# Kernel tuning notes

Hardware: AMD Instinct MI355X
Metric: run time of the kernel (lower is better)

The kernel has to match this reference:

```python
import jax, jax.numpy as jnp
import numpy as np

D_MODEL = 1024
D_KV = 64
N_HEADS = 16
KV_HEADS = 4
G = N_HEADS // KV_HEADS
NUM_BUCKETS = 32
MAX_DISTANCE = 128


def _relative_position_bucket(relative_position, bidirectional=True,
                              num_buckets=NUM_BUCKETS, max_distance=MAX_DISTANCE):
    # Faithful port of T5Attention._relative_position_bucket
    relative_buckets = jnp.zeros_like(relative_position)
    if bidirectional:
        num_buckets //= 2
        relative_buckets = (relative_position > 0).astype(jnp.int32) * num_buckets
        relative_position = jnp.abs(relative_position)
    else:
        relative_position = -jnp.minimum(relative_position, 0)
    max_exact = num_buckets // 2
    is_small = relative_position < max_exact
    rel_if_large = max_exact + (
        jnp.log(relative_position.astype(jnp.float32) / max_exact)
        / np.log(max_distance / max_exact) * (num_buckets - max_exact)
    ).astype(jnp.int32)
    rel_if_large = jnp.minimum(rel_if_large, num_buckets - 1)
    return relative_buckets + jnp.where(is_small, relative_position, rel_if_large)


def setup_inputs() -> dict:
    key = jax.random.key(0)
    ks = jax.random.split(key, 6)
    B, S = 2, 2048
    inner = N_HEADS * D_KV
    sc = 1.0 / np.sqrt(D_MODEL)
    return {
        "hidden_states": jax.random.normal(ks[0], (B, S, D_MODEL), dtype=jnp.float32),
        "Wq": jax.random.normal(ks[1], (D_MODEL, inner), dtype=jnp.float32) * sc,
        "Wk": jax.random.normal(ks[2], (D_MODEL, inner), dtype=jnp.float32) * sc,
        "Wv": jax.random.normal(ks[3], (D_MODEL, inner), dtype=jnp.float32) * sc,
        "Wo": jax.random.normal(ks[4], (inner, D_MODEL), dtype=jnp.float32) * sc,
        "rel_bias": jax.random.normal(ks[5], (NUM_BUCKETS, N_HEADS), dtype=jnp.float32) * 0.1,
    }


def reference(hidden_states, Wq, Wk, Wv, Wo, rel_bias):
    B, S, _ = hidden_states.shape

    def split_heads(x):  # [B,S,inner] -> [B,H,S,Dk]
        return x.reshape(B, S, N_HEADS, D_KV).transpose(0, 2, 1, 3)

    q = split_heads(hidden_states @ Wq)
    k = split_heads(hidden_states @ Wk)
    v = split_heads(hidden_states @ Wv)

    # head index = g * KV_HEADS + h (einops 'b (g h) ...' with h=kv_heads)
    gq = q.reshape(B, G, KV_HEADS, S, D_KV)
    gk = k.reshape(B, G, KV_HEADS, S, D_KV).mean(axis=1)  # [B,Hkv,S,Dk]
    # einsum sums over g (as in torch.einsum 'bghnd,bhsd->bhns'); no 1/sqrt(d) in T5
    scores = jnp.einsum('bghnd,bhsd->bhns', gq, gk)  # [B,Hkv,S,S]

    # T5 relative position bias (bidirectional, encoder)
    ctx = jnp.arange(S)[:, None]
    mem = jnp.arange(S)[None, :]
    buckets = _relative_position_bucket(mem - ctx, bidirectional=True)
    bias = rel_bias[buckets]                # [S,S,H]
    bias = bias.transpose(2, 0, 1)[None]    # [1,H,S,S]
    gbias = bias.reshape(1, G, KV_HEADS, S, S).mean(axis=1)  # [1,Hkv,S,S]

    scores = scores + gbias
    attn = jax.nn.softmax(scores.astype(jnp.float32), axis=-1).astype(scores.dtype)

    # repeat grouped attn weights back to full heads: 'b h n s -> b (g h) n s'
    attn_full = jnp.tile(attn, (1, G, 1, 1))  # [B,H,S,S]
    ctx_out = jnp.einsum('bhns,bhsd->bhnd', attn_full, v)  # [B,H,S,Dk]
    ctx_out = ctx_out.transpose(0, 2, 1, 3).reshape(B, S, N_HEADS * D_KV)
    return ctx_out @ Wo  # [B,S,D_MODEL]
```

## Files before the change

kernel.cpp:

```cpp
#include <hip/hip_runtime.h>
#include <math.h>


typedef __bf16 bf16_t;
typedef bf16_t bf16x8 __attribute__((ext_vector_type(8)));
typedef bf16_t bf16x4 __attribute__((ext_vector_type(4)));
typedef float f32x4 __attribute__((ext_vector_type(4)));

#define MFMA16(a, b, c) __builtin_amdgcn_mfma_f32_16x16x32_bf16(a, b, c, 0, 0, 0)

typedef __attribute__((address_space(1))) void gvoid;
typedef __attribute__((address_space(3))) void svoid;
__device__ __forceinline__ void gld16(const void* g, void* l) {
    __builtin_amdgcn_global_load_lds((gvoid*)g, (svoid*)l, 16, 0, 0);
}

__global__ __launch_bounds__(256) void prep_all(const float* __restrict__ hs,
                                                const float* __restrict__ Wq,
                                                const float* __restrict__ Wk,
                                                const float* __restrict__ Wv,
                                                const float* __restrict__ Wo,
                                                const float* __restrict__ rel_bias,
                                                bf16_t* __restrict__ hs_hi,
                                                bf16_t* __restrict__ hs_lo,
                                                bf16_t* __restrict__ Thi,
                                                bf16_t* __restrict__ Tlo,
                                                bf16_t* __restrict__ WvT,
                                                bf16_t* __restrict__ WoT,
                                                float* __restrict__ btab) {
    __shared__ float sm[2048];
    const int r = blockIdx.x, t = threadIdx.x;
    if (r < 4096) {
        size_t idx = ((size_t)r * 256 + t) * 4;
        float4 v = *(const float4*)(hs + idx);
        bf16x4 h, l;
        h[0] = (bf16_t)v.x; l[0] = (bf16_t)(v.x - (float)h[0]);
        h[1] = (bf16_t)v.y; l[1] = (bf16_t)(v.y - (float)h[1]);
        h[2] = (bf16_t)v.z; l[2] = (bf16_t)(v.z - (float)h[2]);
        h[3] = (bf16_t)v.w; l[3] = (bf16_t)(v.w - (float)h[3]);
        *(bf16x4*)(hs_hi + idx) = h;
        *(bf16x4*)(hs_lo + idx) = l;
    } else if (r < 5120) {
        int k = r - 4096;
        float* rq = sm;
        float* rk = sm + 1024;
#pragma unroll
        for (int j = 0; j < 4; ++j) {
            rq[t + j * 256] = Wq[(size_t)k * 1024 + t + j * 256];
            rk[t + j * 256] = Wk[(size_t)k * 1024 + t + j * 256];
        }
        __syncthreads();
        int h = t >> 6, j2 = t & 63;
        float sq = 0.f, sk = 0.f;
#pragma unroll
        for (int g = 0; g < 4; ++g) {
            sq += rq[(g * 4 + h) * 64 + j2];
            sk += rk[(g * 4 + h) * 64 + j2];
        }
        sk *= 0.25f;
        bf16_t qh = (bf16_t)sq;
        Thi[(size_t)t * 1024 + k] = qh;
        Tlo[(size_t)t * 1024 + k] = (bf16_t)(sq - (float)qh);
        bf16_t kh = (bf16_t)sk;
        Thi[(size_t)(256 + t) * 1024 + k] = kh;
        Tlo[(size_t)(256 + t) * 1024 + k] = (bf16_t)(sk - (float)kh);
    } else if (r < 7168) {
        const float* src = (r < 6144) ? Wv : Wo;
        bf16_t* dst = (r < 6144) ? WvT : WoT;
        int rr = (r < 6144) ? r - 5120 : r - 6144;
        int bx = (rr & 31) * 32, by = (rr >> 5) * 32;
        int tx = t & 31, ty = t >> 5;
        float(*tile)[33] = (float(*)[33])sm;
#pragma unroll
        for (int i = 0; i < 32; i += 8)
            tile[ty + i][tx] = src[(size_t)(by + ty + i) * 1024 + bx + tx];
        __syncthreads();
#pragma unroll
        for (int i = 0; i < 32; i += 8)
            dst[(size_t)(bx + ty + i) * 1024 + by + tx] = (bf16_t)tile[tx][ty + i];
    } else {
        int idx = (r - 7168) * 256 + t;
        if (idx >= 4095) return;
        int delta = idx - 2047;
        int bucket = (delta > 0) ? 16 : 0;
        int arp = delta < 0 ? -delta : delta;
        int rb;
        if (arp < 8) {
            rb = arp;
        } else {
            float tt = (logf((float)arp * 0.125f) / 2.772588722239781f) * 8.0f;
            int ri = 8 + (int)tt;
            rb = ri < 15 ? ri : 15;
        }
        bucket += rb;
#pragma unroll
        for (int h = 0; h < 4; ++h) {
            float s = 0.25f * (rel_bias[bucket * 16 + h] + rel_bias[bucket * 16 + h + 4] +
                               rel_bias[bucket * 16 + h + 8] + rel_bias[bucket * 16 + h + 12]);
            btab[h * 4608 + idx] = s;
        }
    }
}

__global__ __launch_bounds__(256, 1) void proj_qkv(const bf16_t* __restrict__ Ah,
                                                   const bf16_t* __restrict__ Al,
                                                   const bf16_t* __restrict__ Bh,
                                                   const bf16_t* __restrict__ Bl,
                                                   const bf16_t* __restrict__ WvT,
                                                   bf16_t* __restrict__ Qhi,
                                                   bf16_t* __restrict__ Qlo,
                                                   bf16_t* __restrict__ Kbh,
                                                   bf16_t* __restrict__ Kbl,
                                                   bf16_t* __restrict__ Vb) {
    __shared__ bf16_t pool[24576];
    const int K = 1024, nk = 32;
    const int t = threadIdx.x;
    const int w = t >> 6, lane = t & 63;
    const int lr = lane & 15, q = lane >> 4;
    const int bx = blockIdx.x;
    const bool qk = bx < 8;
    const int m0 = blockIdx.y * 128;
    const int n0 = qk ? bx * 64 : (bx - 8) * 128;
    const int mw = (w & 1) * 64;
    f32x4 acc[4][4] = {};

    const int rA = t & 127, cA0 = t >> 7, cA1 = 2 + (t >> 7);
    const size_t oA0 = (size_t)(m0 + rA) * K + cA0 * 8;
    const size_t oA1 = (size_t)(m0 + rA) * K + cA1 * 8;
    const int rBq = t & 63, cBq = t >> 6;
    const size_t oBq = (size_t)(n0 + rBq) * K + cBq * 8;
    const size_t oBv0 = (size_t)(n0 + rA) * K + cA0 * 8;
    const size_t oBv1 = (size_t)(n0 + rA) * K + cA1 * 8;

    auto stage = [&](int bf, int k0) {
        gld16(Ah + oA0 + k0, &pool[bf * 4096 + t * 8]);
        gld16(Ah + oA1 + k0, &pool[bf * 4096 + (256 + t) * 8]);
        if (qk) {
            gld16(Al + oA0 + k0, &pool[8192 + bf * 4096 + t * 8]);
            gld16(Al + oA1 + k0, &pool[8192 + bf * 4096 + (256 + t) * 8]);
            gld16(Bh + oBq + k0, &pool[16384 + bf * 2048 + t * 8]);
            gld16(Bl + oBq + k0, &pool[20480 + bf * 2048 + t * 8]);
        } else {
            gld16(WvT + oBv0 + k0, &pool[8192 + bf * 4096 + t * 8]);
            gld16(WvT + oBv1 + k0, &pool[8192 + bf * 4096 + (256 + t) * 8]);
        }
    };

    stage(0, 0);
    __syncthreads();
    for (int it = 0; it < nk; ++it) {
        const int cur = it & 1;
        if (it + 1 < nk) stage(cur ^ 1, (it + 1) * 32);
        if (qk) {
            const int nw = (w >> 1) * 32;
            bf16x8 ah[4], al[4], bh[2], bl[2];
#pragma unroll
            for (int i = 0; i < 4; ++i) {
                int sa = (q * 128 + mw + i * 16 + lr) * 8;
                ah[i] = *(const bf16x8*)&pool[cur * 4096 + sa];
                al[i] = *(const bf16x8*)&pool[8192 + cur * 4096 + sa];
            }
#pragma unroll
            for (int j = 0; j < 2; ++j) {
                int sb = (q * 64 + nw + j * 16 + lr) * 8;
                bh[j] = *(const bf16x8*)&pool[16384 + cur * 2048 + sb];
                bl[j] = *(const bf16x8*)&pool[20480 + cur * 2048 + sb];
            }
#pragma unroll
            for (int i = 0; i < 4; ++i)
#pragma unroll
                for (int j = 0; j < 2; ++j) {
                    acc[i][j] = MFMA16(ah[i], bh[j], acc[i][j]);
                    acc[i][j] = MFMA16(ah[i], bl[j], acc[i][j]);
                    acc[i][j] = MFMA16(al[i], bh[j], acc[i][j]);
                }
        } else {
            const int nw = (w >> 1) * 64;
            bf16x8 af[4], bfv[4];
#pragma unroll
            for (int i = 0; i < 4; ++i)
                af[i] = *(const bf16x8*)&pool[cur * 4096 + (q * 128 + mw + i * 16 + lr) * 8];
#pragma unroll
            for (int j = 0; j < 4; ++j)
                bfv[j] =
                    *(const bf16x8*)&pool[8192 + cur * 4096 + (q * 128 + nw + j * 16 + lr) * 8];
#pragma unroll
            for (int i = 0; i < 4; ++i)
#pragma unroll
                for (int j = 0; j < 4; ++j) acc[i][j] = MFMA16(af[i], bfv[j], acc[i][j]);
        }
        __syncthreads();
    }

    const int nj = qk ? 2 : 4;
    const int nwq = qk ? (w >> 1) * 32 : (w >> 1) * 64;
#pragma unroll
    for (int i = 0; i < 4; ++i) {
        int row = m0 + mw + i * 16 + q * 4;
#pragma unroll 4
        for (int j = 0; j < nj; ++j) {
            int col = n0 + nwq + j * 16 + lr;
#pragma unroll
            for (int reg = 0; reg < 4; ++reg) {
                float x = acc[i][j][reg];
                int token = row + reg;
                if (qk) {
                    bf16_t hi = (bf16_t)x;
                    bf16_t lo = (bf16_t)(x - (float)hi);
                    if (col < 256) {
                        size_t o = (size_t)token * 256 + col;
                        Qhi[o] = hi;
                        Qlo[o] = lo;
                    } else {
                        int hc = col - 256;
                        int h = hc >> 6, d = hc & 63;
                        int b = token >> 11, s = token & 2047;
                        int it2 = s >> 6, sl = s & 63;
                        size_t o = ((size_t)((b * 4 + h) * 32 + it2)) * 4096 +
                                   (size_t)((d >> 3) * 64 + sl) * 8 + (d & 7);
                        Kbh[o] = hi;
                        Kbl[o] = lo;
                    }
                } else {
                    int vg = col;
                    int h = (vg >> 6) & 3, g = vg >> 8, d = vg & 63;
                    int b = token >> 11, s = token & 2047;
                    int it2 = s >> 6, sc = (s >> 3) & 7, si = s & 7;
                    size_t o = ((size_t)((b * 4 + h) * 32 + it2)) * 16384 +
                               (size_t)(sc * 256 + g * 64 + d) * 8 + si;
                    Vb[o] = (bf16_t)x;
                }
            }
        }
    }
}

__global__ __launch_bounds__(256, 1) void gemm_out(const bf16_t* __restrict__ A,
                                                   const bf16_t* __restrict__ BT,
                                                   float* __restrict__ C,
                                                   int M, int N, int K) {
    __shared__ bf16_t pool[12288];
    const int t = threadIdx.x;
    const int w = t >> 6, lane = t & 63;
    const int lr = lane & 15, q = lane >> 4;
    const int m0 = blockIdx.y * 128, n0 = blockIdx.x * 64;
    const int mw = (w & 1) * 64, nw = (w >> 1) * 32;
    f32x4 acc[4][2] = {};
    const int nk = K >> 5;

    const int rA = t & 127, cA0 = t >> 7, cA1 = 2 + (t >> 7);
    const bf16_t* gA0 = A + (size_t)(m0 + rA) * K + cA0 * 8;
    const bf16_t* gA1 = A + (size_t)(m0 + rA) * K + cA1 * 8;
    const bf16_t* gB = BT + (size_t)(n0 + (t & 63)) * K + (t >> 6) * 8;

    auto stage = [&](int bf, int k0) {
        gld16(gA0 + k0, &pool[bf * 4096 + t * 8]);
        gld16(gA1 + k0, &pool[bf * 4096 + (256 + t) * 8]);
        gld16(gB + k0, &pool[8192 + bf * 2048 + t * 8]);
    };

    stage(0, 0);
    __syncthreads();
    for (int it = 0; it < nk; ++it) {
        const int cur = it & 1;
        if (it + 1 < nk) stage(cur ^ 1, (it + 1) * 32);
        bf16x8 af[4], bfv[2];
#pragma unroll
        for (int i = 0; i < 4; ++i)
            af[i] = *(const bf16x8*)&pool[cur * 4096 + (q * 128 + mw + i * 16 + lr) * 8];
#pragma unroll
        for (int j = 0; j < 2; ++j)
            bfv[j] = *(const bf16x8*)&pool[8192 + cur * 2048 + (q * 64 + nw + j * 16 + lr) * 8];
#pragma unroll
        for (int i = 0; i < 4; ++i)
#pragma unroll
            for (int j = 0; j < 2; ++j) acc[i][j] = MFMA16(af[i], bfv[j], acc[i][j]);
        __syncthreads();
    }

#pragma unroll
    for (int i = 0; i < 4; ++i) {
        int row = m0 + mw + i * 16 + q * 4;
#pragma unroll
        for (int j = 0; j < 2; ++j) {
            int col = n0 + nw + j * 16 + lr;
#pragma unroll
            for (int reg = 0; reg < 4; ++reg)
                C[(size_t)(row + reg) * N + col] = acc[i][j][reg];
        }
    }
}

__global__ __launch_bounds__(512, 1) void attn_mfma(const bf16_t* __restrict__ Qhi,
                                                    const bf16_t* __restrict__ Qlo,
                                                    const bf16_t* __restrict__ Kbh,
                                                    const bf16_t* __restrict__ Kbl,
                                                    const bf16_t* __restrict__ Vb,
                                                    const float* __restrict__ btab,
                                                    bf16_t* __restrict__ part0,
                                                    bf16_t* __restrict__ part1,
                                                    float* __restrict__ Sml) {
    __shared__ bf16_t Kh[2][4096], Kl[2][4096], Vsm[2][16384], Ps[8192];
    const int t = threadIdx.x, w = t >> 6, lane = t & 63;
    const int lr = lane & 15, q = lane >> 4;
    const int blk = blockIdx.x;
    const int half = blk & 1, qt = (blk >> 1) & 15, h = (blk >> 5) & 3, b = blk >> 7;
    const int n0 = qt * 128;
    const int rowbase = n0 + w * 16;
    const int swz = (lr & 7) << 3;
    const int psb = w * 1024 + lr * 64;

    const size_t qrow = (size_t)(b * 2048 + rowbase + lr) * 256 + h * 64;
    bf16x8 aqh[2], aql[2];
#pragma unroll
    for (int kb = 0; kb < 2; ++kb) {
        aqh[kb] = *(const bf16x8*)(Qhi + qrow + kb * 32 + q * 8);
        aql[kb] = *(const bf16x8*)(Qlo + qrow + kb * 32 + q * 8);
    }

    const int tilebase = (b * 4 + h) * 32 + half * 16;
    const bf16_t* gK = Kbh + (size_t)tilebase * 4096;
    const bf16_t* gL = Kbl + (size_t)tilebase * 4096;
    const bf16_t* gV = Vb + (size_t)tilebase * 16384;
    const float* btabh = btab + h * 4608 + 2047;

    auto stage = [&](int bf, int it) {
        gld16(gK + (size_t)it * 4096 + t * 8, &Kh[bf][t * 8]);
        gld16(gL + (size_t)it * 4096 + t * 8, &Kl[bf][t * 8]);
        const bf16_t* v0 = gV + (size_t)it * 16384;
#pragma unroll
        for (int j = 0; j < 4; ++j)
            gld16(v0 + (j * 512 + t) * 8, &Vsm[bf][(j * 512 + t) * 8]);
    };

    float m_r = -INFINITY, l_r = 0.f;
    f32x4 O[16] = {};

    stage(0, 0);
    __syncthreads();
    for (int it = 0; it < 16; ++it) {
        const int cur = it & 1;
        if (it + 1 < 16) stage(cur ^ 1, it + 1);
        const int s0g = half * 1024 + it * 64;

        f32x4 sc[4];
#pragma unroll
        for (int ct = 0; ct < 4; ++ct) {
            f32x4 z = {0.f, 0.f, 0.f, 0.f};
#pragma unroll
            for (int kb = 0; kb < 2; ++kb) {
                int sb = ((kb * 4 + q) * 64 + ct * 16 + lr) * 8;
                bf16x8 bh = *(const bf16x8*)&Kh[cur][sb];
                bf16x8 bl = *(const bf16x8*)&Kl[cur][sb];
                z = MFMA16(bh, aqh[kb], z);
                z = MFMA16(bh, aql[kb], z);
                z = MFMA16(bl, aqh[kb], z);
            }
            sc[ct] = z;
        }
        const int dbase = (s0g + q * 4) - (rowbase + lr);
#pragma unroll
        for (int ct = 0; ct < 4; ++ct)
#pragma unroll
            for (int reg = 0; reg < 4; ++reg)
                sc[ct][reg] += btabh[dbase + ct * 16 + reg];

        float mt = fmaxf(fmaxf(sc[0][0], sc[0][1]), fmaxf(sc[0][2], sc[0][3]));
#pragma unroll
        for (int ct = 1; ct < 4; ++ct)
            mt = fmaxf(mt, fmaxf(fmaxf(sc[ct][0], sc[ct][1]), fmaxf(sc[ct][2], sc[ct][3])));
        mt = fmaxf(mt, __shfl_xor(mt, 16, 64));
        mt = fmaxf(mt, __shfl_xor(mt, 32, 64));

        float mn = fmaxf(m_r, mt);
        float al = __expf(m_r - mn);
        m_r = mn;
        float rs = 0.f;
#pragma unroll
        for (int ct = 0; ct < 4; ++ct) {
            bf16x4 tq;
#pragma unroll
            for (int reg = 0; reg < 4; ++reg) {
                float p = __expf(sc[ct][reg] - mn);
                rs += p;
                tq[reg] = (bf16_t)p;
            }
            *(bf16x4*)&Ps[psb + ((ct * 16 + q * 4) ^ swz)] = tq;
        }
        rs += __shfl_xor(rs, 16, 64);
        rs += __shfl_xor(rs, 32, 64);
        l_r = l_r * al + rs;

        bf16x8 pf0 = *(const bf16x8*)&Ps[psb + ((q * 8) ^ swz)];
        bf16x8 pf1 = *(const bf16x8*)&Ps[psb + ((32 + q * 8) ^ swz)];

#pragma unroll
        for (int nt = 0; nt < 16; ++nt) {
            f32x4 o = O[nt];
#pragma unroll
            for (int reg = 0; reg < 4; ++reg) o[reg] *= al;
            bf16x8 v0 = *(const bf16x8*)&Vsm[cur][(q * 256 + nt * 16 + lr) * 8];
            o = MFMA16(v0, pf0, o);
            bf16x8 v1 = *(const bf16x8*)&Vsm[cur][((4 + q) * 256 + nt * 16 + lr) * 8];
            o = MFMA16(v1, pf1, o);
            O[nt] = o;
        }
        __syncthreads();
    }

    bf16_t* P = half ? part1 : part0;
    const float inv = 1.f / l_r;
    const int tokb = b * 2048 + rowbase;
#pragma unroll
    for (int G = 0; G < 4; ++G) {
#pragma unroll
        for (int g4 = 0; g4 < 4; ++g4) {
            int nt = G * 4 + g4;
            bf16x4 tq;
#pragma unroll
            for (int reg = 0; reg < 4; ++reg) tq[reg] = (bf16_t)(O[nt][reg] * inv);
            *(bf16x4*)&Ps[psb + ((g4 * 16 + q * 4) ^ swz)] = tq;
        }
#pragma unroll
        for (int i = 0; i < 2; ++i) {
            int row = i * 8 + (lane >> 3), cv = (lane & 7) * 8;
            bf16x8 fr = *(const bf16x8*)&Ps[w * 1024 + row * 64 + (cv ^ ((row & 7) << 3))];
            *(bf16x8*)(P + (size_t)(tokb + row) * 1024 + (G * 4 + h) * 64 + cv) = fr;
        }
    }
    if (lane < 16)
        Sml[half * 16384 + (size_t)(tokb + lane) * 4 + h] = m_r + logf(l_r);
}

__global__ __launch_bounds__(256) void combine_halves(bf16_t* __restrict__ p0,
                                                      const bf16_t* __restrict__ p1,
                                                      const float* __restrict__ Sml) {
    size_t flat = ((size_t)blockIdx.x * 256 + threadIdx.x) * 8;
    int tok = (int)(flat >> 10), c = (int)(flat & 1023), h = (c >> 6) & 3;
    float s0 = Sml[tok * 4 + h], s1 = Sml[16384 + tok * 4 + h];
    float M = fmaxf(s0, s1);
    float e0 = __expf(s0 - M), e1 = __expf(s1 - M);
    float r = 1.f / (e0 + e1);
    float w0 = e0 * r, w1 = e1 * r;
    bf16x8 a = *(bf16x8*)(p0 + flat);
    bf16x8 bb = *(const bf16x8*)(p1 + flat);
    bf16x8 o;
#pragma unroll
    for (int i = 0; i < 8; ++i) o[i] = (bf16_t)(w0 * (float)a[i] + w1 * (float)bb[i]);
    *(bf16x8*)(p0 + flat) = o;
}

extern "C" void kernel_launch(void* const* d_in, const int* in_sizes, int n_in,
                              void* d_out, int out_size, void* d_ws, size_t ws_size,
                              hipStream_t stream) {
    const float* hs = (const float*)d_in[0];
    const float* Wq = (const float*)d_in[1];
    const float* Wk = (const float*)d_in[2];
    const float* Wv = (const float*)d_in[3];
    const float* Wo = (const float*)d_in[4];
    const float* rb = (const float*)d_in[5];
    float* out = (float*)d_out;

    const size_t MB = 1 << 20;
    const size_t KB = 1 << 10;
    char* ws = (char*)d_ws;
    bf16_t* hs_hi = (bf16_t*)(ws);
    bf16_t* hs_lo = (bf16_t*)(ws + 8 * MB);
    bf16_t* WqkThi = (bf16_t*)(ws + 16 * MB);
    bf16_t* WqkTlo = (bf16_t*)(ws + 17 * MB);
    bf16_t* WvT = (bf16_t*)(ws + 18 * MB);
    bf16_t* WoT = (bf16_t*)(ws + 20 * MB);
    float* btab = (float*)(ws + 22 * MB);
    float* Sml = (float*)(ws + 22 * MB + 128 * KB);
    bf16_t* Qhi = (bf16_t*)(ws + 22 * MB + 256 * KB);
    bf16_t* Qlo = Qhi + (size_t)4096 * 256;
    bf16_t* Kbh = Qlo + (size_t)4096 * 256;
    bf16_t* Kbl = Kbh + (size_t)4096 * 256;
    bf16_t* Vb = Kbl + (size_t)4096 * 256;
    bf16_t* part0 = hs_hi;
    bf16_t* part1 = hs_lo;

    prep_all<<<7184, 256, 0, stream>>>(hs, Wq, Wk, Wv, Wo, rb, hs_hi, hs_lo, WqkThi,
                                       WqkTlo, WvT, WoT, btab);
    proj_qkv<<<dim3(16, 32), 256, 0, stream>>>(hs_hi, hs_lo, WqkThi, WqkTlo, WvT, Qhi,
                                               Qlo, Kbh, Kbl, Vb);
    attn_mfma<<<256, 512, 0, stream>>>(Qhi, Qlo, Kbh, Kbl, Vb, btab, part0, part1, Sml);
    combine_halves<<<2048, 256, 0, stream>>>(part0, part1, Sml);
    gemm_out<<<dim3(16, 32), 256, 0, stream>>>(part0, WoT, out, 4096, 1024, 1024);
}
```

Baseline: 229.5 us.

## Triple-buffer LDS staging in projection GEMMs with fine-grained vmcnt waits

```diff
diff --git a/kernel.cpp b/kernel.cpp
--- a/kernel.cpp
+++ b/kernel.cpp
@@ -112,7 +112,7 @@
                                                    bf16_t* __restrict__ Kbh,
                                                    bf16_t* __restrict__ Kbl,
                                                    bf16_t* __restrict__ Vb) {
-    __shared__ bf16_t pool[24576];
+    __shared__ bf16_t pool[36864];
     const int K = 1024, nk = 32;
     const int t = threadIdx.x;
     const int w = t >> 6, lane = t & 63;
@@ -132,40 +132,57 @@
     const size_t oBv0 = (size_t)(n0 + rA) * K + cA0 * 8;
     const size_t oBv1 = (size_t)(n0 + rA) * K + cA1 * 8;
 
-    auto stage = [&](int bf, int k0) {
-        gld16(Ah + oA0 + k0, &pool[bf * 4096 + t * 8]);
-        gld16(Ah + oA1 + k0, &pool[bf * 4096 + (256 + t) * 8]);
+    auto stage = [&](int bf, int kidx) {
+        const int k0 = kidx * 32;
+        bf16_t* base = &pool[bf * 12288];
+        gld16(Ah + oA0 + k0, base + t * 8);
+        gld16(Ah + oA1 + k0, base + (256 + t) * 8);
         if (qk) {
-            gld16(Al + oA0 + k0, &pool[8192 + bf * 4096 + t * 8]);
-            gld16(Al + oA1 + k0, &pool[8192 + bf * 4096 + (256 + t) * 8]);
-            gld16(Bh + oBq + k0, &pool[16384 + bf * 2048 + t * 8]);
-            gld16(Bl + oBq + k0, &pool[20480 + bf * 2048 + t * 8]);
+            gld16(Al + oA0 + k0, base + 4096 + t * 8);
+            gld16(Al + oA1 + k0, base + 4096 + (256 + t) * 8);
+            gld16(Bh + oBq + k0, base + 8192 + t * 8);
+            gld16(Bl + oBq + k0, base + 10240 + t * 8);
         } else {
-            gld16(WvT + oBv0 + k0, &pool[8192 + bf * 4096 + t * 8]);
-            gld16(WvT + oBv1 + k0, &pool[8192 + bf * 4096 + (256 + t) * 8]);
+            gld16(WvT + oBv0 + k0, base + 4096 + t * 8);
+            gld16(WvT + oBv1 + k0, base + 4096 + (256 + t) * 8);
         }
     };
 
     stage(0, 0);
-    __syncthreads();
+    stage(1, 1);
+    stage(2, 2);
+    if (qk)
+        asm volatile("s_waitcnt vmcnt(12)" ::: "memory");
+    else
+        asm volatile("s_waitcnt vmcnt(8)" ::: "memory");
+    __builtin_amdgcn_s_barrier();
+
     for (int it = 0; it < nk; ++it) {
-        const int cur = it & 1;
-        if (it + 1 < nk) stage(cur ^ 1, (it + 1) * 32);
+        const int cur = it % 3;
+        const bf16_t* base = &pool[cur * 12288];
         if (qk) {
             const int nw = (w >> 1) * 32;
             bf16x8 ah[4], al[4], bh[2], bl[2];
 #pragma unroll
             for (int i = 0; i < 4; ++i) {
                 int sa = (q * 128 + mw + i * 16 + lr) * 8;
-                ah[i] = *(const bf16x8*)&pool[cur * 4096 + sa];
-                al[i] = *(const bf16x8*)&pool[8192 + cur * 4096 + sa];
+                ah[i] = *(const bf16x8*)&base[sa];
+                al[i] = *(const bf16x8*)&base[4096 + sa];
             }
 #pragma unroll
             for (int j = 0; j < 2; ++j) {
                 int sb = (q * 64 + nw + j * 16 + lr) * 8;
-                bh[j] = *(const bf16x8*)&pool[16384 + cur * 2048 + sb];
-                bl[j] = *(const bf16x8*)&pool[20480 + cur * 2048 + sb];
+                bh[j] = *(const bf16x8*)&base[8192 + sb];
+                bl[j] = *(const bf16x8*)&base[10240 + sb];
             }
+            asm volatile("s_waitcnt lgkmcnt(0)" ::: "memory");
+            if (it + 2 < nk)
+                asm volatile("s_waitcnt vmcnt(6)" ::: "memory");
+            else
+                asm volatile("s_waitcnt vmcnt(0)" ::: "memory");
+            __builtin_amdgcn_s_barrier();
+            if (it + 3 < nk) stage(cur, it + 3);
+            __builtin_amdgcn_sched_barrier(0);
 #pragma unroll
             for (int i = 0; i < 4; ++i)
 #pragma unroll
@@ -179,17 +196,23 @@
             bf16x8 af[4], bfv[4];
 #pragma unroll
             for (int i = 0; i < 4; ++i)
-                af[i] = *(const bf16x8*)&pool[cur * 4096 + (q * 128 + mw + i * 16 + lr) * 8];
+                af[i] = *(const bf16x8*)&base[(q * 128 + mw + i * 16 + lr) * 8];
 #pragma unroll
             for (int j = 0; j < 4; ++j)
-                bfv[j] =
-                    *(const bf16x8*)&pool[8192 + cur * 4096 + (q * 128 + nw + j * 16 + lr) * 8];
+                bfv[j] = *(const bf16x8*)&base[4096 + (q * 128 + nw + j * 16 + lr) * 8];
+            asm volatile("s_waitcnt lgkmcnt(0)" ::: "memory");
+            if (it + 2 < nk)
+                asm volatile("s_waitcnt vmcnt(4)" ::: "memory");
+            else
+                asm volatile("s_waitcnt vmcnt(0)" ::: "memory");
+            __builtin_amdgcn_s_barrier();
+            if (it + 3 < nk) stage(cur, it + 3);
+            __builtin_amdgcn_sched_barrier(0);
 #pragma unroll
             for (int i = 0; i < 4; ++i)
 #pragma unroll
                 for (int j = 0; j < 4; ++j) acc[i][j] = MFMA16(af[i], bfv[j], acc[i][j]);
         }
-        __syncthreads();
     }
 
     const int nj = qk ? 2 : 4;
@@ -239,7 +262,7 @@
                                                    const bf16_t* __restrict__ BT,
                                                    float* __restrict__ C,
                                                    int M, int N, int K) {
-    __shared__ bf16_t pool[12288];
+    __shared__ bf16_t pool[18432];
     const int t = threadIdx.x;
     const int w = t >> 6, lane = t & 63;
     const int lr = lane & 15, q = lane >> 4;
@@ -253,29 +276,42 @@
     const bf16_t* gA1 = A + (size_t)(m0 + rA) * K + cA1 * 8;
     const bf16_t* gB = BT + (size_t)(n0 + (t & 63)) * K + (t >> 6) * 8;
 
-    auto stage = [&](int bf, int k0) {
-        gld16(gA0 + k0, &pool[bf * 4096 + t * 8]);
-        gld16(gA1 + k0, &pool[bf * 4096 + (256 + t) * 8]);
-        gld16(gB + k0, &pool[8192 + bf * 2048 + t * 8]);
+    auto stage = [&](int bf, int kidx) {
+        const int k0 = kidx * 32;
+        bf16_t* base = &pool[bf * 6144];
+        gld16(gA0 + k0, base + t * 8);
+        gld16(gA1 + k0, base + (256 + t) * 8);
+        gld16(gB + k0, base + 4096 + t * 8);
     };
 
     stage(0, 0);
-    __syncthreads();
+    stage(1, 1);
+    stage(2, 2);
+    asm volatile("s_waitcnt vmcnt(6)" ::: "memory");
+    __builtin_amdgcn_s_barrier();
+
     for (int it = 0; it < nk; ++it) {
-        const int cur = it & 1;
-        if (it + 1 < nk) stage(cur ^ 1, (it + 1) * 32);
+        const int cur = it % 3;
+        const bf16_t* base = &pool[cur * 6144];
         bf16x8 af[4], bfv[2];
 #pragma unroll
         for (int i = 0; i < 4; ++i)
-            af[i] = *(const bf16x8*)&pool[cur * 4096 + (q * 128 + mw + i * 16 + lr) * 8];
+            af[i] = *(const bf16x8*)&base[(q * 128 + mw + i * 16 + lr) * 8];
 #pragma unroll
         for (int j = 0; j < 2; ++j)
-            bfv[j] = *(const bf16x8*)&pool[8192 + cur * 2048 + (q * 64 + nw + j * 16 + lr) * 8];
+            bfv[j] = *(const bf16x8*)&base[4096 + (q * 64 + nw + j * 16 + lr) * 8];
+        asm volatile("s_waitcnt lgkmcnt(0)" ::: "memory");
+        if (it + 2 < nk)
+            asm volatile("s_waitcnt vmcnt(3)" ::: "memory");
+        else
+            asm volatile("s_waitcnt vmcnt(0)" ::: "memory");
+        __builtin_amdgcn_s_barrier();
+        if (it + 3 < nk) stage(cur, it + 3);
+        __builtin_amdgcn_sched_barrier(0);
 #pragma unroll
         for (int i = 0; i < 4; ++i)
 #pragma unroll
             for (int j = 0; j < 2; ++j) acc[i][j] = MFMA16(af[i], bfv[j], acc[i][j]);
-        __syncthreads();
     }
 
 #pragma unroll
```

Measured after the change: 243.8 us. +6.2%, slower.

## Remap block indices for XCD-aware L2 locality and vectorize V stores

Applied to the files above, without the earlier changes.

```diff
diff --git a/kernel.cpp b/kernel.cpp
--- a/kernel.cpp
+++ b/kernel.cpp
@@ -117,9 +117,11 @@
     const int t = threadIdx.x;
     const int w = t >> 6, lane = t & 63;
     const int lr = lane & 15, q = lane >> 4;
-    const int bx = blockIdx.x;
+    const int l = blockIdx.y * 16 + blockIdx.x;
+    const int nl = (l & 7) * 64 + (l >> 3);
+    const int bx = nl & 15;
+    const int m0 = (nl >> 4) * 128;
     const bool qk = bx < 8;
-    const int m0 = blockIdx.y * 128;
     const int n0 = qk ? bx * 64 : (bx - 8) * 128;
     const int mw = (w & 1) * 64;
     f32x4 acc[4][4] = {};
@@ -192,19 +194,18 @@
         __syncthreads();
     }
 
-    const int nj = qk ? 2 : 4;
-    const int nwq = qk ? (w >> 1) * 32 : (w >> 1) * 64;
-#pragma unroll
-    for (int i = 0; i < 4; ++i) {
-        int row = m0 + mw + i * 16 + q * 4;
-#pragma unroll 4
-        for (int j = 0; j < nj; ++j) {
-            int col = n0 + nwq + j * 16 + lr;
-#pragma unroll
-            for (int reg = 0; reg < 4; ++reg) {
-                float x = acc[i][j][reg];
-                int token = row + reg;
-                if (qk) {
+    if (qk) {
+        const int nwq = (w >> 1) * 32;
+#pragma unroll
+        for (int i = 0; i < 4; ++i) {
+            int row = m0 + mw + i * 16 + q * 4;
+#pragma unroll
+            for (int j = 0; j < 2; ++j) {
+                int col = n0 + nwq + j * 16 + lr;
+#pragma unroll
+                for (int reg = 0; reg < 4; ++reg) {
+                    float x = acc[i][j][reg];
+                    int token = row + reg;
                     bf16_t hi = (bf16_t)x;
                     bf16_t lo = (bf16_t)(x - (float)hi);
                     if (col < 256) {
@@ -213,23 +214,34 @@
                         Qlo[o] = lo;
                     } else {
                         int hc = col - 256;
-                        int h = hc >> 6, d = hc & 63;
+                        int hh = hc >> 6, d = hc & 63;
                         int b = token >> 11, s = token & 2047;
                         int it2 = s >> 6, sl = s & 63;
-                        size_t o = ((size_t)((b * 4 + h) * 32 + it2)) * 4096 +
+                        size_t o = ((size_t)((b * 4 + hh) * 32 + it2)) * 4096 +
                                    (size_t)((d >> 3) * 64 + sl) * 8 + (d & 7);
                         Kbh[o] = hi;
                         Kbl[o] = lo;
                     }
-                } else {
-                    int vg = col;
-                    int h = (vg >> 6) & 3, g = vg >> 8, d = vg & 63;
-                    int b = token >> 11, s = token & 2047;
-                    int it2 = s >> 6, sc = (s >> 3) & 7, si = s & 7;
-                    size_t o = ((size_t)((b * 4 + h) * 32 + it2)) * 16384 +
-                               (size_t)(sc * 256 + g * 64 + d) * 8 + si;
-                    Vb[o] = (bf16_t)x;
                 }
+            }
+        }
+    } else {
+        const int nwq = (w >> 1) * 64;
+#pragma unroll
+        for (int i = 0; i < 4; ++i) {
+            int row = m0 + mw + i * 16 + q * 4;
+            int b = row >> 11, s = row & 2047;
+            int it2 = s >> 6, sc2 = (s >> 3) & 7, si = s & 7;
+#pragma unroll
+            for (int j = 0; j < 4; ++j) {
+                int col = n0 + nwq + j * 16 + lr;
+                int hh = (col >> 6) & 3, g = col >> 8, d = col & 63;
+                size_t o = ((size_t)((b * 4 + hh) * 32 + it2)) * 16384 +
+                           (size_t)(sc2 * 256 + g * 64 + d) * 8 + si;
+                bf16x4 pv;
+#pragma unroll
+                for (int reg = 0; reg < 4; ++reg) pv[reg] = (bf16_t)acc[i][j][reg];
+                *(bf16x4*)(Vb + o) = pv;
             }
         }
     }
@@ -243,7 +255,9 @@
     const int t = threadIdx.x;
     const int w = t >> 6, lane = t & 63;
     const int lr = lane & 15, q = lane >> 4;
-    const int m0 = blockIdx.y * 128, n0 = blockIdx.x * 64;
+    const int l = blockIdx.y * 16 + blockIdx.x;
+    const int nl = (l & 7) * 64 + (l >> 3);
+    const int m0 = (nl >> 4) * 128, n0 = (nl & 15) * 64;
     const int mw = (w & 1) * 64, nw = (w >> 1) * 32;
     f32x4 acc[4][2] = {};
     const int nk = K >> 5;
@@ -303,7 +317,8 @@
     __shared__ bf16_t Kh[2][4096], Kl[2][4096], Vsm[2][16384], Ps[8192];
     const int t = threadIdx.x, w = t >> 6, lane = t & 63;
     const int lr = lane & 15, q = lane >> 4;
-    const int blk = blockIdx.x;
+    const int bl0 = blockIdx.x;
+    const int blk = (bl0 & 7) * 32 + (bl0 >> 3);
     const int half = blk & 1, qt = (blk >> 1) & 15, h = (blk >> 5) & 3, b = blk >> 7;
     const int n0 = qt * 128;
     const int rowbase = n0 + w * 16;
```

Result: faster. 223.3 us (-2.7%).
